# Optimization experiments

Measured on AMD Instinct MI355X. Metric: run time of the kernel, lower is better.

The kernel has to match this reference:

```python
import jax, jax.numpy as jnp
import numpy as np

N_HEAD = 16

def setup_inputs() -> dict:
    key = jax.random.key(0)
    k1, k2, k3 = jax.random.split(key, 3)
    B, T, C = 4, 2048, 1024
    x = jax.random.normal(k1, (B, T, C), dtype=jnp.float32)
    w_qkv = jax.random.normal(k2, (C, 3 * C), dtype=jnp.float32) * (C ** -0.5)
    w_out = jax.random.normal(k3, (C, C), dtype=jnp.float32) * (C ** -0.5)
    return {"x": x, "w_qkv": w_qkv, "w_out": w_out}

def reference(x, w_qkv, w_out):
    B, T, C = x.shape
    H = N_HEAD
    d_k = C // H
    scale = d_k ** -0.5
    qkv = (x @ w_qkv).reshape(B, T, 3, H, d_k)
    q = qkv[:, :, 0].transpose(0, 2, 1, 3)  # [B,H,T,d_k]
    k = qkv[:, :, 1].transpose(0, 2, 1, 3)
    v = qkv[:, :, 2].transpose(0, 2, 1, 3)
    scores = jnp.einsum('bhqd,bhkd->bhqk', q, k) * scale  # [B,H,T,T]
    causal = jnp.tril(jnp.ones((T, T), dtype=bool))
    scores = jnp.where(causal[None, None], scores, jnp.finfo(scores.dtype).min)
    probs = jax.nn.softmax(scores, axis=-1)
    out = jnp.einsum('bhqk,bhkd->bhqd', probs, v)  # [B,H,T,d_k]
    out = out.transpose(0, 2, 1, 3).reshape(B, T, C)
    return out @ w_out
```

## Files before the change

### kernel.cpp

```cpp
#include <hip/hip_runtime.h>
#include <stdint.h>


typedef __bf16 bf16_t;
typedef __bf16 bf16x4 __attribute__((ext_vector_type(4)));
typedef __bf16 bf16x8 __attribute__((ext_vector_type(8)));
typedef float f32x4 __attribute__((ext_vector_type(4)));

#define LOG2E 1.44269504088896340736f
#define QSCALE (0.125f * LOG2E)

__device__ __forceinline__ void gl_lds16(const void* g, void* l) {
  __builtin_amdgcn_global_load_lds(
      (const __attribute__((address_space(1))) unsigned int*)g,
      (__attribute__((address_space(3))) unsigned int*)l, 16, 0, 0);
}

__device__ __forceinline__ f32x4 mfma16(bf16x8 a, bf16x8 b, f32x4 c) {
  return __builtin_amdgcn_mfma_f32_16x16x32_bf16(a, b, c, 0, 0, 0);
}

__global__ __launch_bounds__(256) void k_cvt_bf16(const float* __restrict__ in,
                                                  bf16_t* __restrict__ out, int n4) {
  int i = blockIdx.x * 256 + threadIdx.x;
  int step = gridDim.x * 256;
  for (; i < n4; i += step) {
    f32x4 v = reinterpret_cast<const f32x4*>(in)[i];
    bf16x4 o;
    o[0] = (bf16_t)v[0]; o[1] = (bf16_t)v[1];
    o[2] = (bf16_t)v[2]; o[3] = (bf16_t)v[3];
    reinterpret_cast<bf16x4*>(out)[i] = o;
  }
}

__global__ __launch_bounds__(256) void k_transpose_cvt(const float* __restrict__ in,
                                                       bf16_t* __restrict__ out,
                                                       int R, int Cc) {
  __shared__ float tile[64][65];
  const int tid = threadIdx.x;
  const int c0 = blockIdx.x * 64, r0 = blockIdx.y * 64;
  const int rr = tid >> 4, cc = (tid & 15) * 4;
#pragma unroll
  for (int i = 0; i < 4; i++) {
    f32x4 v = *reinterpret_cast<const f32x4*>(&in[(size_t)(r0 + rr + i * 16) * Cc + c0 + cc]);
    tile[rr + i * 16][cc + 0] = v[0];
    tile[rr + i * 16][cc + 1] = v[1];
    tile[rr + i * 16][cc + 2] = v[2];
    tile[rr + i * 16][cc + 3] = v[3];
  }
  __syncthreads();
  const int cr = tid >> 2, kb = (tid & 3) * 16;
#pragma unroll
  for (int j4 = 0; j4 < 4; j4++) {
    bf16x4 o;
#pragma unroll
    for (int jj = 0; jj < 4; jj++) o[jj] = (bf16_t)tile[kb + j4 * 4 + jj][cr];
    *reinterpret_cast<bf16x4*>(&out[(size_t)(c0 + cr) * R + r0 + kb + j4 * 4]) = o;
  }
}

template <int MODE>
__global__ __launch_bounds__(256) void k_gemm(const bf16_t* __restrict__ A,
                                              const bf16_t* __restrict__ Bt,
                                              void* __restrict__ C0, void* __restrict__ C1,
                                              int M, int N, int K, int nbx) {
  constexpr int BM = 128, BN = 128, BK = 32;
  __shared__ bf16_t a_sh[2][BM * BK];
  __shared__ bf16_t b_sh[2][BN * BK];
  const int tid = threadIdx.x;
  const int wave = tid >> 6, lane = tid & 63;
  const int g = lane >> 4, lr = lane & 15;
  const int wm = wave >> 1, wn = wave & 1;
  const int nblk = gridDim.x;
  const int swid = (blockIdx.x & 7) * (nblk >> 3) + (blockIdx.x >> 3);
  const int m0 = (swid / nbx) * BM, n0 = (swid % nbx) * BN;
  const bf16_t* Ab = A + (size_t)m0 * K;
  const bf16_t* Bb = Bt + (size_t)n0 * K;

  f32x4 acc[4][4];
#pragma unroll
  for (int i = 0; i < 4; i++)
#pragma unroll
    for (int j = 0; j < 4; j++) acc[i][j] = (f32x4){0.f, 0.f, 0.f, 0.f};

  auto stage = [&](int buf, int k0) {
#pragma unroll
    for (int i = 0; i < 2; i++) {
      int c = tid + 256 * i;
      gl_lds16(Ab + (size_t)(c >> 2) * K + k0 + (c & 3) * 8, &a_sh[buf][c * 8]);
    }
#pragma unroll
    for (int i = 0; i < 2; i++) {
      int c = tid + 256 * i;
      gl_lds16(Bb + (size_t)(c >> 2) * K + k0 + (c & 3) * 8, &b_sh[buf][c * 8]);
    }
  };

  stage(0, 0);
  __syncthreads();
  int cur = 0;
  for (int k0 = 0; k0 < K; k0 += BK) {
    if (k0 + BK < K) stage(cur ^ 1, k0 + BK);
    bf16x8 af[4], bfr[4];
#pragma unroll
    for (int mi = 0; mi < 4; mi++)
      af[mi] = *reinterpret_cast<const bf16x8*>(&a_sh[cur][(wm * 64 + mi * 16 + lr) * BK + g * 8]);
#pragma unroll
    for (int ni = 0; ni < 4; ni++)
      bfr[ni] = *reinterpret_cast<const bf16x8*>(&b_sh[cur][(wn * 64 + ni * 16 + lr) * BK + g * 8]);
    __builtin_amdgcn_s_setprio(1);
#pragma unroll
    for (int mi = 0; mi < 4; mi++)
#pragma unroll
      for (int ni = 0; ni < 4; ni++) acc[mi][ni] = mfma16(af[mi], bfr[ni], acc[mi][ni]);
    __builtin_amdgcn_s_setprio(0);
    __syncthreads();
    cur ^= 1;
  }

#pragma unroll
  for (int mi = 0; mi < 4; mi++) {
#pragma unroll
    for (int ni = 0; ni < 4; ni++) {
      const int mb = m0 + wm * 64 + mi * 16 + g * 4;
      const int nb = n0 + wn * 64 + ni * 16;
      if constexpr (MODE == 2) {
        float* C = (float*)C0;
#pragma unroll
        for (int r = 0; r < 4; r++) C[(size_t)(mb + r) * N + nb + lr] = acc[mi][ni][r];
      } else {
        if (nb < 2048) {
          const float scl = (nb < 1024) ? QSCALE : 1.0f;
          bf16_t* qk = (bf16_t*)C0;
#pragma unroll
          for (int r = 0; r < 4; r++)
            qk[(size_t)(mb + r) * 2048 + nb + lr] = (bf16_t)(acc[mi][ni][r] * scl);
        } else {
          bf16_t* vT = (bf16_t*)C1;
          const int b = mb >> 11, t = mb & 2047;
          const int col = nb - 2048 + lr;
          const int h = col >> 6, d = col & 63;
          bf16x4 o;
#pragma unroll
          for (int r = 0; r < 4; r++) o[r] = (bf16_t)acc[mi][ni][r];
          *reinterpret_cast<bf16x4*>(&vT[((size_t)(b * 16 + h) * 64 + d) * 2048 + t]) = o;
        }
      }
    }
  }
}

__global__ __launch_bounds__(256) void k_attn(const bf16_t* __restrict__ qk,
                                              const bf16_t* __restrict__ vT,
                                              bf16_t* __restrict__ out) {
  constexpr int T = 2048;
  constexpr int PST = 72;
  __shared__ bf16_t k_sh[2][64 * 64];
  __shared__ bf16_t v_sh[2][64 * 64];
  __shared__ bf16_t p_sh[4][32 * PST];
  const int tid = threadIdx.x;
  const int wave = tid >> 6, lane = tid & 63;
  const int g = lane >> 4, lr = lane & 15;

  const int flat = blockIdx.x;
  const int qt = 15 - (flat >> 6);
  const int s6 = flat & 63;
  const int bh = (s6 & 7) * 8 + (s6 >> 3);
  const int b = bh >> 4, h = bh & 15;
  const int q0w = qt * 128 + wave * 32;

  bf16x8 qf[2][2];
#pragma unroll
  for (int rb = 0; rb < 2; rb++) {
    const bf16_t* Qr = qk + (size_t)(b * T + q0w + rb * 16 + lr) * 2048 + h * 64;
    qf[rb][0] = *reinterpret_cast<const bf16x8*>(Qr + g * 8);
    qf[rb][1] = *reinterpret_cast<const bf16x8*>(Qr + 32 + g * 8);
  }

  f32x4 acc_o[2][4];
#pragma unroll
  for (int rb = 0; rb < 2; rb++)
#pragma unroll
    for (int dt = 0; dt < 4; dt++) acc_o[rb][dt] = (f32x4){0.f, 0.f, 0.f, 0.f};
  float mrow[2] = {-1e30f, -1e30f};
  float lrow[2] = {0.f, 0.f};

  const int nt = 2 * qt + 2;
  const bf16_t* Kbase = qk + (size_t)b * T * 2048 + 1024 + h * 64;
  const bf16_t* Vbase = vT + (size_t)bh * 64 * T;

  auto stageK = [&](int buf, int kv) {
#pragma unroll
    for (int i = 0; i < 2; i++) {
      int c = tid + 256 * i;
      int row = c >> 3, col8 = (c & 7) ^ (row & 7);
      gl_lds16(Kbase + (size_t)(kv + row) * 2048 + col8 * 8, &k_sh[buf][c * 8]);
    }
#pragma unroll
    for (int i = 0; i < 2; i++) {
      int c = tid + 256 * i;
      int d = c >> 3, col8 = (c & 7) ^ (d & 7);
      gl_lds16(Vbase + (size_t)d * T + kv + col8 * 8, &v_sh[buf][c * 8]);
    }
  };

  stageK(0, 0);
  __syncthreads();

  int cur = 0;
  for (int t = 0; t < nt; ++t) {
    const int kv0 = t * 64;
    if (t + 1 < nt) stageK(cur ^ 1, kv0 + 64);

    f32x4 s[2][4];
#pragma unroll
    for (int rb = 0; rb < 2; rb++)
#pragma unroll
      for (int kt = 0; kt < 4; kt++) s[rb][kt] = (f32x4){0.f, 0.f, 0.f, 0.f};
    __builtin_amdgcn_s_setprio(1);
#pragma unroll
    for (int kt = 0; kt < 4; kt++) {
      const int row = kt * 16 + lr, sw = row & 7;
      bf16x8 kf0 = *reinterpret_cast<const bf16x8*>(&k_sh[cur][row * 64 + (g ^ sw) * 8]);
      bf16x8 kf1 = *reinterpret_cast<const bf16x8*>(&k_sh[cur][row * 64 + ((4 + g) ^ sw) * 8]);
#pragma unroll
      for (int rb = 0; rb < 2; rb++) {
        s[rb][kt] = mfma16(kf0, qf[rb][0], s[rb][kt]);
        s[rb][kt] = mfma16(kf1, qf[rb][1], s[rb][kt]);
      }
    }
    __builtin_amdgcn_s_setprio(0);

    if (kv0 + 63 > q0w) {
#pragma unroll
      for (int rb = 0; rb < 2; rb++)
#pragma unroll
        for (int kt = 0; kt < 4; kt++)
#pragma unroll
          for (int r = 0; r < 4; r++)
            if (kv0 + kt * 16 + g * 4 + r > q0w + rb * 16 + lr) s[rb][kt][r] = -1e30f;
    }

#pragma unroll
    for (int rb = 0; rb < 2; rb++) {
      float pm = s[rb][0][0];
#pragma unroll
      for (int kt = 0; kt < 4; kt++)
#pragma unroll
        for (int r = 0; r < 4; r++) pm = fmaxf(pm, s[rb][kt][r]);
      pm = fmaxf(pm, __shfl_xor(pm, 16, 64));
      pm = fmaxf(pm, __shfl_xor(pm, 32, 64));

      unsigned long long need = __ballot(pm > mrow[rb] + 8.0f);
      if (need) {
        float mnew = fmaxf(mrow[rb], pm);
        float alpha = __builtin_amdgcn_exp2f(mrow[rb] - mnew);
        mrow[rb] = mnew;
        lrow[rb] *= alpha;
#pragma unroll
        for (int r = 0; r < 4; r++) {
          int src = (lane & 48) | ((lane >> 2) & 12) | r;
          float ar = __shfl(alpha, src, 64);
#pragma unroll
          for (int dt = 0; dt < 4; dt++) acc_o[rb][dt][r] *= ar;
        }
      }

      float rs = 0.f;
#pragma unroll
      for (int kt = 0; kt < 4; kt++) {
        f32x4 p;
#pragma unroll
        for (int r = 0; r < 4; r++) p[r] = __builtin_amdgcn_exp2f(s[rb][kt][r] - mrow[rb]);
        rs += (p[0] + p[1]) + (p[2] + p[3]);
        bf16x4 pb;
#pragma unroll
        for (int r = 0; r < 4; r++) pb[r] = (bf16_t)p[r];
        *reinterpret_cast<bf16x4*>(&p_sh[wave][(rb * 16 + lr) * PST + kt * 16 + g * 4]) = pb;
      }
      rs += __shfl_xor(rs, 16, 64);
      rs += __shfl_xor(rs, 32, 64);
      lrow[rb] += rs;
    }

    bf16x8 pa[2][2];
#pragma unroll
    for (int rb = 0; rb < 2; rb++) {
      pa[rb][0] = *reinterpret_cast<const bf16x8*>(&p_sh[wave][(rb * 16 + lr) * PST + g * 8]);
      pa[rb][1] = *reinterpret_cast<const bf16x8*>(&p_sh[wave][(rb * 16 + lr) * PST + 32 + g * 8]);
    }
    __builtin_amdgcn_s_setprio(1);
#pragma unroll
    for (int dt = 0; dt < 4; dt++) {
      const int drow = dt * 16 + lr, sw = drow & 7;
      bf16x8 v0 = *reinterpret_cast<const bf16x8*>(&v_sh[cur][drow * 64 + (g ^ sw) * 8]);
      bf16x8 v1 = *reinterpret_cast<const bf16x8*>(&v_sh[cur][drow * 64 + ((4 + g) ^ sw) * 8]);
#pragma unroll
      for (int rb = 0; rb < 2; rb++) {
        acc_o[rb][dt] = mfma16(pa[rb][0], v0, acc_o[rb][dt]);
        acc_o[rb][dt] = mfma16(pa[rb][1], v1, acc_o[rb][dt]);
      }
    }
    __builtin_amdgcn_s_setprio(0);

    __syncthreads();
    cur ^= 1;
  }

#pragma unroll
  for (int rb = 0; rb < 2; rb++) {
    const float linv = 1.0f / lrow[rb];
#pragma unroll
    for (int r = 0; r < 4; r++) {
      int src = (lane & 48) | ((lane >> 2) & 12) | r;
      float lq = __shfl(linv, src, 64);
#pragma unroll
      for (int dt = 0; dt < 4; dt++)
        out[(size_t)(b * T + q0w + rb * 16 + g * 4 + r) * 1024 + h * 64 + dt * 16 + lr] =
            (bf16_t)(acc_o[rb][dt][r] * lq);
    }
  }
}

extern "C" void kernel_launch(void* const* d_in, const int* in_sizes, int n_in,
                              void* d_out, int out_size, void* d_ws, size_t ws_size,
                              hipStream_t stream) {
  (void)in_sizes; (void)n_in; (void)out_size; (void)ws_size;
  const float* x = (const float*)d_in[0];
  const float* w_qkv = (const float*)d_in[1];
  const float* w_out = (const float*)d_in[2];
  float* out = (float*)d_out;
  const int T = 2048, C = 1024;
  const int M = 4 * T;

  bf16_t* xb = (bf16_t*)d_ws;
  bf16_t* wqkvT = xb + (size_t)M * C;
  bf16_t* woutT = wqkvT + (size_t)3 * C * C;
  bf16_t* qkbuf = woutT + (size_t)C * C;
  bf16_t* vT = qkbuf + (size_t)M * 2 * C;
  bf16_t* attn = vT + (size_t)M * C;

  k_cvt_bf16<<<2048, 256, 0, stream>>>(x, xb, M * C / 4);
  k_transpose_cvt<<<dim3(3 * C / 64, C / 64), 256, 0, stream>>>(w_qkv, wqkvT, C, 3 * C);
  k_transpose_cvt<<<dim3(C / 64, C / 64), 256, 0, stream>>>(w_out, woutT, C, C);
  k_gemm<1><<<(3 * C / 128) * (M / 128), 256, 0, stream>>>(xb, wqkvT, qkbuf, vT, M, 3 * C, C,
                                                           3 * C / 128);
  k_attn<<<1024, 256, 0, stream>>>(qkbuf, vT, attn);
  k_gemm<2><<<(C / 128) * (M / 128), 256, 0, stream>>>(attn, woutT, out, nullptr, M, C, C,
                                                       C / 128);
}
```

Before: 256.2 us.

## Move V transpose to separate kernel, use incremental load pointers, skip masked tiles

The QKV GEMM now writes V row-major with coalesced stores, and a new LDS-based kernel transposes it into the per-head layout that attention reads. This replaces the scattered strided 4-element transposed stores in the GEMM epilogue, at the cost of an extra launch and an extra read and write pass over V. The GEMM and attention loaders now precompute per-thread global pointers and advance them by a fixed stride each iteration, which cuts address arithmetic. Attention waves whose 32 query rows lie entirely before the current KV tile skip the compute while still joining the shared loads and barriers. The attention output buffer is moved to reuse the V row-major buffer.

Result: no change. 259.9 us (+1.4%).

```diff
diff --git a/kernel.cpp b/kernel.cpp
--- a/kernel.cpp
+++ b/kernel.cpp
@@ -56,6 +56,38 @@
 #pragma unroll
     for (int jj = 0; jj < 4; jj++) o[jj] = (bf16_t)tile[kb + j4 * 4 + jj][cr];
     *reinterpret_cast<bf16x4*>(&out[(size_t)(c0 + cr) * R + r0 + kb + j4 * 4]) = o;
+  }
+}
+
+__global__ __launch_bounds__(256) void k_transpose_v(const bf16_t* __restrict__ v,
+                                                     bf16_t* __restrict__ vT) {
+  __shared__ bf16_t tile[64 * 64];
+  const int tid = threadIdx.x;
+  const int bh = blockIdx.y;
+  const int b = bh >> 4, h = bh & 15;
+  const int t0 = blockIdx.x * 64;
+#pragma unroll
+  for (int i = 0; i < 2; i++) {
+    int c = tid + 256 * i;
+    int tl = c >> 3, ch = c & 7;
+    bf16x8 val = *reinterpret_cast<const bf16x8*>(
+        &v[(size_t)(b * 2048 + t0 + tl) * 1024 + h * 64 + ch * 8]);
+    int sw = (ch ^ (tl & 7) ^ (tl >> 3)) & 7;
+    *reinterpret_cast<bf16x8*>(&tile[tl * 64 + sw * 8]) = val;
+  }
+  __syncthreads();
+#pragma unroll
+  for (int i = 0; i < 2; i++) {
+    int c = tid + 256 * i;
+    int d = c >> 3, tc = c & 7;
+    bf16x8 o;
+#pragma unroll
+    for (int j = 0; j < 8; j++) {
+      int t = tc * 8 + j;
+      int sw = ((d >> 3) ^ (t & 7) ^ (t >> 3)) & 7;
+      o[j] = tile[t * 64 + sw * 8 + (d & 7)];
+    }
+    *reinterpret_cast<bf16x8*>(&vT[((size_t)bh * 64 + d) * 2048 + t0 + tc * 8]) = o;
   }
 }
 
@@ -74,8 +106,15 @@
   const int nblk = gridDim.x;
   const int swid = (blockIdx.x & 7) * (nblk >> 3) + (blockIdx.x >> 3);
   const int m0 = (swid / nbx) * BM, n0 = (swid % nbx) * BN;
-  const bf16_t* Ab = A + (size_t)m0 * K;
-  const bf16_t* Bb = Bt + (size_t)n0 * K;
+
+  const bf16_t* ag[2];
+  const bf16_t* bg[2];
+#pragma unroll
+  for (int i = 0; i < 2; i++) {
+    int c = tid + 256 * i;
+    ag[i] = A + (size_t)(m0 + (c >> 2)) * K + (c & 3) * 8;
+    bg[i] = Bt + (size_t)(n0 + (c >> 2)) * K + (c & 3) * 8;
+  }
 
   f32x4 acc[4][4];
 #pragma unroll
@@ -83,24 +122,22 @@
 #pragma unroll
     for (int j = 0; j < 4; j++) acc[i][j] = (f32x4){0.f, 0.f, 0.f, 0.f};
 
-  auto stage = [&](int buf, int k0) {
-#pragma unroll
-    for (int i = 0; i < 2; i++) {
-      int c = tid + 256 * i;
-      gl_lds16(Ab + (size_t)(c >> 2) * K + k0 + (c & 3) * 8, &a_sh[buf][c * 8]);
-    }
-#pragma unroll
-    for (int i = 0; i < 2; i++) {
-      int c = tid + 256 * i;
-      gl_lds16(Bb + (size_t)(c >> 2) * K + k0 + (c & 3) * 8, &b_sh[buf][c * 8]);
-    }
-  };
-
-  stage(0, 0);
+#pragma unroll
+  for (int i = 0; i < 2; i++) {
+    gl_lds16(ag[i], &a_sh[0][(tid + 256 * i) * 8]);
+    gl_lds16(bg[i], &b_sh[0][(tid + 256 * i) * 8]);
+  }
   __syncthreads();
   int cur = 0;
   for (int k0 = 0; k0 < K; k0 += BK) {
-    if (k0 + BK < K) stage(cur ^ 1, k0 + BK);
+    if (k0 + BK < K) {
+#pragma unroll
+      for (int i = 0; i < 2; i++) {
+        ag[i] += BK; bg[i] += BK;
+        gl_lds16(ag[i], &a_sh[cur ^ 1][(tid + 256 * i) * 8]);
+        gl_lds16(bg[i], &b_sh[cur ^ 1][(tid + 256 * i) * 8]);
+      }
+    }
     bf16x8 af[4], bfr[4];
 #pragma unroll
     for (int mi = 0; mi < 4; mi++)
@@ -136,14 +173,10 @@
           for (int r = 0; r < 4; r++)
             qk[(size_t)(mb + r) * 2048 + nb + lr] = (bf16_t)(acc[mi][ni][r] * scl);
         } else {
-          bf16_t* vT = (bf16_t*)C1;
-          const int b = mb >> 11, t = mb & 2047;
-          const int col = nb - 2048 + lr;
-          const int h = col >> 6, d = col & 63;
-          bf16x4 o;
-#pragma unroll
-          for (int r = 0; r < 4; r++) o[r] = (bf16_t)acc[mi][ni][r];
-          *reinterpret_cast<bf16x4*>(&vT[((size_t)(b * 16 + h) * 64 + d) * 2048 + t]) = o;
+          bf16_t* vb = (bf16_t*)C1;
+#pragma unroll
+          for (int r = 0; r < 4; r++)
+            vb[(size_t)(mb + r) * 1024 + (nb - 2048) + lr] = (bf16_t)acc[mi][ni][r];
         }
       }
     }
@@ -186,122 +219,134 @@
   float lrow[2] = {0.f, 0.f};
 
   const int nt = 2 * qt + 2;
-  const bf16_t* Kbase = qk + (size_t)b * T * 2048 + 1024 + h * 64;
-  const bf16_t* Vbase = vT + (size_t)bh * 64 * T;
-
-  auto stageK = [&](int buf, int kv) {
+
+  const bf16_t* kg[2];
+  const bf16_t* vg[2];
+  {
+    const bf16_t* Kbase = qk + (size_t)b * T * 2048 + 1024 + h * 64;
+    const bf16_t* Vbase = vT + (size_t)bh * 64 * T;
 #pragma unroll
     for (int i = 0; i < 2; i++) {
       int c = tid + 256 * i;
       int row = c >> 3, col8 = (c & 7) ^ (row & 7);
-      gl_lds16(Kbase + (size_t)(kv + row) * 2048 + col8 * 8, &k_sh[buf][c * 8]);
-    }
-#pragma unroll
-    for (int i = 0; i < 2; i++) {
-      int c = tid + 256 * i;
-      int d = c >> 3, col8 = (c & 7) ^ (d & 7);
-      gl_lds16(Vbase + (size_t)d * T + kv + col8 * 8, &v_sh[buf][c * 8]);
-    }
-  };
-
-  stageK(0, 0);
+      kg[i] = Kbase + (size_t)row * 2048 + col8 * 8;
+      vg[i] = Vbase + (size_t)row * T + col8 * 8;
+    }
+  }
+
+#pragma unroll
+  for (int i = 0; i < 2; i++) {
+    gl_lds16(kg[i], &k_sh[0][(tid + 256 * i) * 8]);
+    gl_lds16(vg[i], &v_sh[0][(tid + 256 * i) * 8]);
+  }
   __syncthreads();
 
   int cur = 0;
   for (int t = 0; t < nt; ++t) {
     const int kv0 = t * 64;
-    if (t + 1 < nt) stageK(cur ^ 1, kv0 + 64);
-
-    f32x4 s[2][4];
-#pragma unroll
-    for (int rb = 0; rb < 2; rb++)
-#pragma unroll
-      for (int kt = 0; kt < 4; kt++) s[rb][kt] = (f32x4){0.f, 0.f, 0.f, 0.f};
-    __builtin_amdgcn_s_setprio(1);
-#pragma unroll
-    for (int kt = 0; kt < 4; kt++) {
-      const int row = kt * 16 + lr, sw = row & 7;
-      bf16x8 kf0 = *reinterpret_cast<const bf16x8*>(&k_sh[cur][row * 64 + (g ^ sw) * 8]);
-      bf16x8 kf1 = *reinterpret_cast<const bf16x8*>(&k_sh[cur][row * 64 + ((4 + g) ^ sw) * 8]);
+    if (t + 1 < nt) {
+#pragma unroll
+      for (int i = 0; i < 2; i++) {
+        kg[i] += 64 * 2048;
+        vg[i] += 64;
+        gl_lds16(kg[i], &k_sh[cur ^ 1][(tid + 256 * i) * 8]);
+        gl_lds16(vg[i], &v_sh[cur ^ 1][(tid + 256 * i) * 8]);
+      }
+    }
+
+    if (kv0 <= q0w + 31) {
+      f32x4 s[2][4];
+#pragma unroll
+      for (int rb = 0; rb < 2; rb++)
+#pragma unroll
+        for (int kt = 0; kt < 4; kt++) s[rb][kt] = (f32x4){0.f, 0.f, 0.f, 0.f};
+      __builtin_amdgcn_s_setprio(1);
+#pragma unroll
+      for (int kt = 0; kt < 4; kt++) {
+        const int row = kt * 16 + lr, sw = row & 7;
+        bf16x8 kf0 = *reinterpret_cast<const bf16x8*>(&k_sh[cur][row * 64 + (g ^ sw) * 8]);
+        bf16x8 kf1 = *reinterpret_cast<const bf16x8*>(&k_sh[cur][row * 64 + ((4 + g) ^ sw) * 8]);
+#pragma unroll
+        for (int rb = 0; rb < 2; rb++) {
+          s[rb][kt] = mfma16(kf0, qf[rb][0], s[rb][kt]);
+          s[rb][kt] = mfma16(kf1, qf[rb][1], s[rb][kt]);
+        }
+      }
+      __builtin_amdgcn_s_setprio(0);
+
+      if (kv0 + 63 > q0w) {
+#pragma unroll
+        for (int rb = 0; rb < 2; rb++)
+#pragma unroll
+          for (int kt = 0; kt < 4; kt++)
+#pragma unroll
+            for (int r = 0; r < 4; r++)
+              if (kv0 + kt * 16 + g * 4 + r > q0w + rb * 16 + lr) s[rb][kt][r] = -1e30f;
+      }
+
 #pragma unroll
       for (int rb = 0; rb < 2; rb++) {
-        s[rb][kt] = mfma16(kf0, qf[rb][0], s[rb][kt]);
-        s[rb][kt] = mfma16(kf1, qf[rb][1], s[rb][kt]);
-      }
-    }
-    __builtin_amdgcn_s_setprio(0);
-
-    if (kv0 + 63 > q0w) {
-#pragma unroll
-      for (int rb = 0; rb < 2; rb++)
+        float pm = s[rb][0][0];
 #pragma unroll
         for (int kt = 0; kt < 4; kt++)
 #pragma unroll
-          for (int r = 0; r < 4; r++)
-            if (kv0 + kt * 16 + g * 4 + r > q0w + rb * 16 + lr) s[rb][kt][r] = -1e30f;
-    }
-
-#pragma unroll
-    for (int rb = 0; rb < 2; rb++) {
-      float pm = s[rb][0][0];
-#pragma unroll
-      for (int kt = 0; kt < 4; kt++)
-#pragma unroll
-        for (int r = 0; r < 4; r++) pm = fmaxf(pm, s[rb][kt][r]);
-      pm = fmaxf(pm, __shfl_xor(pm, 16, 64));
-      pm = fmaxf(pm, __shfl_xor(pm, 32, 64));
-
-      unsigned long long need = __ballot(pm > mrow[rb] + 8.0f);
-      if (need) {
-        float mnew = fmaxf(mrow[rb], pm);
-        float alpha = __builtin_amdgcn_exp2f(mrow[rb] - mnew);
-        mrow[rb] = mnew;
-        lrow[rb] *= alpha;
-#pragma unroll
-        for (int r = 0; r < 4; r++) {
-          int src = (lane & 48) | ((lane >> 2) & 12) | r;
-          float ar = __shfl(alpha, src, 64);
-#pragma unroll
-          for (int dt = 0; dt < 4; dt++) acc_o[rb][dt][r] *= ar;
-        }
-      }
-
-      float rs = 0.f;
-#pragma unroll
-      for (int kt = 0; kt < 4; kt++) {
-        f32x4 p;
-#pragma unroll
-        for (int r = 0; r < 4; r++) p[r] = __builtin_amdgcn_exp2f(s[rb][kt][r] - mrow[rb]);
-        rs += (p[0] + p[1]) + (p[2] + p[3]);
-        bf16x4 pb;
-#pragma unroll
-        for (int r = 0; r < 4; r++) pb[r] = (bf16_t)p[r];
-        *reinterpret_cast<bf16x4*>(&p_sh[wave][(rb * 16 + lr) * PST + kt * 16 + g * 4]) = pb;
-      }
-      rs += __shfl_xor(rs, 16, 64);
-      rs += __shfl_xor(rs, 32, 64);
-      lrow[rb] += rs;
-    }
-
-    bf16x8 pa[2][2];
-#pragma unroll
-    for (int rb = 0; rb < 2; rb++) {
-      pa[rb][0] = *reinterpret_cast<const bf16x8*>(&p_sh[wave][(rb * 16 + lr) * PST + g * 8]);
-      pa[rb][1] = *reinterpret_cast<const bf16x8*>(&p_sh[wave][(rb * 16 + lr) * PST + 32 + g * 8]);
-    }
-    __builtin_amdgcn_s_setprio(1);
-#pragma unroll
-    for (int dt = 0; dt < 4; dt++) {
-      const int drow = dt * 16 + lr, sw = drow & 7;
-      bf16x8 v0 = *reinterpret_cast<const bf16x8*>(&v_sh[cur][drow * 64 + (g ^ sw) * 8]);
-      bf16x8 v1 = *reinterpret_cast<const bf16x8*>(&v_sh[cur][drow * 64 + ((4 + g) ^ sw) * 8]);
+          for (int r = 0; r < 4; r++) pm = fmaxf(pm, s[rb][kt][r]);
+        pm = fmaxf(pm, __shfl_xor(pm, 16, 64));
+        pm = fmaxf(pm, __shfl_xor(pm, 32, 64));
+
+        unsigned long long need = __ballot(pm > mrow[rb] + 8.0f);
+        if (need) {
+          float mnew = fmaxf(mrow[rb], pm);
+          float alpha = __builtin_amdgcn_exp2f(mrow[rb] - mnew);
+          mrow[rb] = mnew;
+          lrow[rb] *= alpha;
+#pragma unroll
+          for (int r = 0; r < 4; r++) {
+            int src = (lane & 48) | ((lane >> 2) & 12) | r;
+            float ar = __shfl(alpha, src, 64);
+#pragma unroll
+            for (int dt = 0; dt < 4; dt++) acc_o[rb][dt][r] *= ar;
+          }
+        }
+
+        float rs = 0.f;
+#pragma unroll
+        for (int kt = 0; kt < 4; kt++) {
+          f32x4 p;
+#pragma unroll
+          for (int r = 0; r < 4; r++) p[r] = __builtin_amdgcn_exp2f(s[rb][kt][r] - mrow[rb]);
+          rs += (p[0] + p[1]) + (p[2] + p[3]);
+          bf16x4 pb;
+#pragma unroll
+          for (int r = 0; r < 4; r++) pb[r] = (bf16_t)p[r];
+          *reinterpret_cast<bf16x4*>(&p_sh[wave][(rb * 16 + lr) * PST + kt * 16 + g * 4]) = pb;
+        }
+        rs += __shfl_xor(rs, 16, 64);
+        rs += __shfl_xor(rs, 32, 64);
+        lrow[rb] += rs;
+      }
+
+      bf16x8 pa[2][2];
 #pragma unroll
       for (int rb = 0; rb < 2; rb++) {
-        acc_o[rb][dt] = mfma16(pa[rb][0], v0, acc_o[rb][dt]);
-        acc_o[rb][dt] = mfma16(pa[rb][1], v1, acc_o[rb][dt]);
-      }
-    }
-    __builtin_amdgcn_s_setprio(0);
+        pa[rb][0] = *reinterpret_cast<const bf16x8*>(&p_sh[wave][(rb * 16 + lr) * PST + g * 8]);
+        pa[rb][1] =
+            *reinterpret_cast<const bf16x8*>(&p_sh[wave][(rb * 16 + lr) * PST + 32 + g * 8]);
+      }
+      __builtin_amdgcn_s_setprio(1);
+#pragma unroll
+      for (int dt = 0; dt < 4; dt++) {
+        const int drow = dt * 16 + lr, sw = drow & 7;
+        bf16x8 v0 = *reinterpret_cast<const bf16x8*>(&v_sh[cur][drow * 64 + (g ^ sw) * 8]);
+        bf16x8 v1 = *reinterpret_cast<const bf16x8*>(&v_sh[cur][drow * 64 + ((4 + g) ^ sw) * 8]);
+#pragma unroll
+        for (int rb = 0; rb < 2; rb++) {
+          acc_o[rb][dt] = mfma16(pa[rb][0], v0, acc_o[rb][dt]);
+          acc_o[rb][dt] = mfma16(pa[rb][1], v1, acc_o[rb][dt]);
+        }
+      }
+      __builtin_amdgcn_s_setprio(0);
+    }
 
     __syncthreads();
     cur ^= 1;
@@ -337,15 +382,16 @@
   bf16_t* wqkvT = xb + (size_t)M * C;
   bf16_t* woutT = wqkvT + (size_t)3 * C * C;
   bf16_t* qkbuf = woutT + (size_t)C * C;
-  bf16_t* vT = qkbuf + (size_t)M * 2 * C;
-  bf16_t* attn = vT + (size_t)M * C;
+  bf16_t* vbuf = qkbuf + (size_t)M * 2 * C;
+  bf16_t* vT = vbuf + (size_t)M * C;
 
   k_cvt_bf16<<<2048, 256, 0, stream>>>(x, xb, M * C / 4);
   k_transpose_cvt<<<dim3(3 * C / 64, C / 64), 256, 0, stream>>>(w_qkv, wqkvT, C, 3 * C);
   k_transpose_cvt<<<dim3(C / 64, C / 64), 256, 0, stream>>>(w_out, woutT, C, C);
-  k_gemm<1><<<(3 * C / 128) * (M / 128), 256, 0, stream>>>(xb, wqkvT, qkbuf, vT, M, 3 * C, C,
+  k_gemm<1><<<(3 * C / 128) * (M / 128), 256, 0, stream>>>(xb, wqkvT, qkbuf, vbuf, M, 3 * C, C,
                                                            3 * C / 128);
-  k_attn<<<1024, 256, 0, stream>>>(qkbuf, vT, attn);
-  k_gemm<2><<<(C / 128) * (M / 128), 256, 0, stream>>>(attn, woutT, out, nullptr, M, C, C,
+  k_transpose_v<<<dim3(32, 64), 256, 0, stream>>>(vbuf, vT);
+  k_attn<<<1024, 256, 0, stream>>>(qkbuf, vT, vbuf);
+  k_gemm<2><<<(C / 128) * (M / 128), 256, 0, stream>>>(vbuf, woutT, out, nullptr, M, C, C,
                                                        C / 128);
 }
```
